# Kernel optimization log

Hardware: AMD Instinct MI355X
Metric: run time of the kernel (lower is better)

Reference implementation:

```python
import jax, jax.numpy as jnp
import numpy as np

N, D, E, H = 16384, 1024, 4, 4096
TEMP = 1.0

def setup_inputs() -> dict:
    key = jax.random.key(0)
    ks = jax.random.split(key, 6)
    s_in = 1.0 / np.sqrt(D)
    s_h = 1.0 / np.sqrt(H)
    s_g = 1.0 / np.sqrt(2 * D)
    return {
        "q": jax.random.normal(ks[0], (N, D), jnp.float32),
        "k": jax.random.normal(ks[1], (N, D), jnp.float32),
        "W1": jax.random.normal(ks[2], (E, D, H), jnp.float32) * s_in,
        "b1": jnp.zeros((E, H), jnp.float32),
        "W2": jax.random.normal(ks[3], (E, H, D), jnp.float32) * s_h,
        "b2": jnp.zeros((E, D), jnp.float32),
        "Wg": jax.random.normal(ks[4], (2 * D, 4), jnp.float32) * s_g,
        "bg": jnp.zeros((4,), jnp.float32),
    }

def reference(q, k, W1, b1, W2, b2, Wg, bg):
    # Run all E experts on the same tokens via batched GEMMs.
    h = jax.nn.relu(jnp.einsum('nd,edh->neh', q, W1) + b1)        # [N,E,H]
    q_pred = jnp.einsum('neh,ehd->ned', h, W2) + b2               # [N,E,D]
    # Gate: Linear(dim*2 -> 4) on concat(q,k), softmax over experts.
    logits = (jnp.concatenate([q, k], axis=-1) @ Wg + bg) / TEMP  # [N,4]
    gate = jax.nn.softmax(logits, axis=-1)                        # [N,E]
    return jnp.einsum('ned,ne->nd', q_pred, gate)                 # [N,D]
```

## Files before the change

### kernel.cpp

```cpp
#include <hip/hip_runtime.h>
#include <hip/hip_bf16.h>

#define N_TOK 16384
#define DIM   1024
#define NEXP  4
#define HID   4096
#define CHK   8192

typedef __attribute__((ext_vector_type(8))) short short8;
typedef __attribute__((ext_vector_type(4))) short short4v;
typedef __attribute__((ext_vector_type(4))) float float4v;

static __device__ __forceinline__ short f2bf(float f) {
  __hip_bfloat16 h = __float2bfloat16(f);
  return *reinterpret_cast<short*>(&h);
}

#define GLOAD_LDS16(gsrc, ldst)                                                            \
  __builtin_amdgcn_global_load_lds((const __attribute__((address_space(1))) void*)(gsrc),  \
                                   (__attribute__((address_space(3))) void*)(ldst), 16, 0, 0)

__global__ void gatecvt_kernel(const float* __restrict__ q, const float* __restrict__ k,
                               const float* __restrict__ Wg, const float* __restrict__ bg,
                               float* __restrict__ gate, short* __restrict__ qb) {
  const int wave = threadIdx.x >> 6, lane = threadIdx.x & 63;
  const int n = blockIdx.x * 4 + wave;
  const float* qr = q + (size_t)n * DIM;
  const float* kr = k + (size_t)n * DIM;
  short* qbr = qb + (size_t)n * DIM;
  float s0 = 0.f, s1 = 0.f, s2 = 0.f, s3 = 0.f;
#pragma unroll
  for (int it = 0; it < 4; ++it) {
    int d = it * 256 + lane * 4;
    float4 qv = *(const float4*)(qr + d);
    float4 kv = *(const float4*)(kr + d);
    short4v o;
    o[0] = f2bf(qv.x); o[1] = f2bf(qv.y); o[2] = f2bf(qv.z); o[3] = f2bf(qv.w);
    *(short4v*)(qbr + d) = o;
    const float xq[4] = {qv.x, qv.y, qv.z, qv.w};
    const float xk[4] = {kv.x, kv.y, kv.z, kv.w};
#pragma unroll
    for (int j = 0; j < 4; ++j) {
      float4 w = *(const float4*)(Wg + (size_t)(d + j) * 4);
      s0 += xq[j] * w.x; s1 += xq[j] * w.y; s2 += xq[j] * w.z; s3 += xq[j] * w.w;
      float4 w2 = *(const float4*)(Wg + (size_t)(DIM + d + j) * 4);
      s0 += xk[j] * w2.x; s1 += xk[j] * w2.y; s2 += xk[j] * w2.z; s3 += xk[j] * w2.w;
    }
  }
  for (int off = 32; off; off >>= 1) {
    s0 += __shfl_xor(s0, off);
    s1 += __shfl_xor(s1, off);
    s2 += __shfl_xor(s2, off);
    s3 += __shfl_xor(s3, off);
  }
  if (lane == 0) {
    float l0 = s0 + bg[0], l1 = s1 + bg[1], l2 = s2 + bg[2], l3 = s3 + bg[3];
    float m = fmaxf(fmaxf(l0, l1), fmaxf(l2, l3));
    float e0 = expf(l0 - m), e1 = expf(l1 - m), e2 = expf(l2 - m), e3 = expf(l3 - m);
    float inv = 1.f / (e0 + e1 + e2 + e3);
    float4 g; g.x = e0 * inv; g.y = e1 * inv; g.z = e2 * inv; g.w = e3 * inv;
    *(float4*)(gate + (size_t)n * 4) = g;
  }
}

__global__ void transpose_bf16_kernel(const float* __restrict__ in, short* __restrict__ out,
                                      int R, int C) {
  __shared__ float tile[64][65];
  const size_t eoff = (size_t)blockIdx.z * (size_t)R * C;
  const float* src = in + eoff;
  short* dst = out + eoff;
  const int r0 = blockIdx.y * 64, c0 = blockIdx.x * 64;
  const int tc = threadIdx.x & 63, tr = threadIdx.x >> 6;
#pragma unroll
  for (int p = 0; p < 16; ++p) {
    int r = p * 4 + tr;
    tile[r][tc] = src[(size_t)(r0 + r) * C + (c0 + tc)];
  }
  __syncthreads();
#pragma unroll
  for (int p = 0; p < 16; ++p) {
    int i = p * 4 + tr;
    dst[(size_t)(c0 + i) * R + (r0 + tc)] = f2bf(tile[tc][i]);
  }
}

template <int MODE>
__device__ __forceinline__ void gemm_body(short* sA, short* sB,
                                          const short* __restrict__ A, const short* __restrict__ Bt,
                                          int K, int NTM, int NTN, int bid,
                                          const float* __restrict__ bias,
                                          const float* __restrict__ gate4,
                                          short* __restrict__ OutB, float* __restrict__ FOut,
                                          int ldc, int accumulate) {
  int tile_m, tile_n;
  {
    const int m_own = NTM >> 3;
    const int xcd = bid & 7;
    const int idx = bid >> 3;
    const int mgrp = (m_own < 8) ? m_own : 8;
    const int per = mgrp * 4;
    const int pos = idx % per;
    const int chunk = idx / per;
    const int ml = pos % mgrp;
    const int nl = pos / mgrp;
    const int nchunks = NTN >> 2;
    const int nc = chunk % nchunks;
    const int mg2 = chunk / nchunks;
    tile_m = xcd * m_own + mg2 * mgrp + ml;
    tile_n = nc * 4 + nl;
  }
  const int m0 = tile_m * 128;
  const int n0 = tile_n * 128;

  const int t = threadIdx.x;
  const int lane = t & 63;
  const int wave = t >> 6;
  const int wm = (wave >> 1) * 64;
  const int wn = (wave & 1) * 64;
  const int r16 = lane & 15;
  const int kg = lane >> 4;

  float4v acc[4][4];
#pragma unroll
  for (int m = 0; m < 4; ++m)
#pragma unroll
    for (int n = 0; n < 4; ++n) acc[m][n] = (float4v)0.0f;

  for (int k0 = 0; k0 < K; k0 += 64) {
#pragma unroll
    for (int i = 0; i < 4; ++i) {
      int c = i * 256 + t;
      int row = c >> 3;
      int jc = (c & 7) ^ (row & 7);
      GLOAD_LDS16(A + (size_t)(m0 + row) * K + k0 + jc * 8, &sA[c * 8]);
      GLOAD_LDS16(Bt + (size_t)(n0 + row) * K + k0 + jc * 8, &sB[c * 8]);
    }
    __syncthreads();
#pragma unroll
    for (int kk = 0; kk < 2; ++kk) {
      short8 af[4], bfr[4];
#pragma unroll
      for (int m = 0; m < 4; ++m) {
        int row = wm + m * 16 + r16;
        int jc = (kk * 4 + kg) ^ (row & 7);
        af[m] = *(const short8*)&sA[row * 64 + jc * 8];
      }
#pragma unroll
      for (int n = 0; n < 4; ++n) {
        int row = wn + n * 16 + r16;
        int jc = (kk * 4 + kg) ^ (row & 7);
        bfr[n] = *(const short8*)&sB[row * 64 + jc * 8];
      }
#pragma unroll
      for (int m = 0; m < 4; ++m)
#pragma unroll
        for (int n = 0; n < 4; ++n)
          acc[m][n] = __builtin_amdgcn_mfma_f32_16x16x32_bf16(af[m], bfr[n], acc[m][n], 0, 0, 0);
    }
    __syncthreads();
  }

#pragma unroll
  for (int m = 0; m < 4; ++m) {
    int rbase = m0 + wm + m * 16 + kg * 4;
#pragma unroll
    for (int n = 0; n < 4; ++n) {
      int col = n0 + wn + n * 16 + r16;
      float bcol = bias[col];
#pragma unroll
      for (int r = 0; r < 4; ++r) {
        int grow = rbase + r;
        float g = gate4[(size_t)grow * 4];
        float v = acc[m][n][r];
        if (MODE == 1) {
          v += bcol;
          v = fmaxf(v, 0.f);
          v *= g;
          OutB[(size_t)grow * ldc + col] = f2bf(v);
        } else {
          v += g * bcol;
          size_t oi = (size_t)grow * ldc + col;
          if (accumulate) v += FOut[oi];
          FOut[oi] = v;
        }
      }
    }
  }
}

__global__ __launch_bounds__(256, 2)
void fused_kernel(const short* __restrict__ g1A, const short* __restrict__ g1B,
                  const float* __restrict__ g1bias, const float* __restrict__ g1gate,
                  short* __restrict__ g1out,
                  const short* __restrict__ g2A, const short* __restrict__ g2B,
                  const float* __restrict__ g2bias, const float* __restrict__ g2gate,
                  float* __restrict__ g2out, int g2accum, int g2n) {
  __shared__ short sA[128 * 64];
  __shared__ short sB[128 * 64];
  if ((int)blockIdx.x < g2n) {
    gemm_body<2>(sA, sB, g2A, g2B, HID, CHK / 128, DIM / 128, blockIdx.x,
                 g2bias, g2gate, nullptr, g2out, DIM, g2accum);
  } else {
    gemm_body<1>(sA, sB, g1A, g1B, DIM, CHK / 128, HID / 128, blockIdx.x - g2n,
                 g1bias, g1gate, g1out, nullptr, HID, 0);
  }
}

template <int MODE>
__global__ __launch_bounds__(256, 2)
void gemm_kernel(const short* __restrict__ A, const short* __restrict__ Bt, int K, int NTN,
                 const float* __restrict__ bias, const float* __restrict__ gate4,
                 short* __restrict__ OutB, float* __restrict__ FOut, int ldc, int accumulate) {
  __shared__ short sA[128 * 64];
  __shared__ short sB[128 * 64];
  gemm_body<MODE>(sA, sB, A, Bt, K, gridDim.x / NTN, NTN, blockIdx.x,
                  bias, gate4, OutB, FOut, ldc, accumulate);
}

extern "C" void kernel_launch(void* const* d_in, const int* in_sizes, int n_in,
                              void* d_out, int out_size, void* d_ws, size_t ws_size,
                              hipStream_t stream) {
  const float* q  = (const float*)d_in[0];
  const float* k  = (const float*)d_in[1];
  const float* W1 = (const float*)d_in[2];
  const float* b1 = (const float*)d_in[3];
  const float* W2 = (const float*)d_in[4];
  const float* b2 = (const float*)d_in[5];
  const float* Wg = (const float*)d_in[6];
  const float* bg = (const float*)d_in[7];
  float* out = (float*)d_out;

  char* ws = (char*)d_ws;
  size_t off = 0;
  float* gate = (float*)(ws + off); off += (size_t)N_TOK * 4 * sizeof(float);
  short* qb   = (short*)(ws + off); off += (size_t)N_TOK * DIM * 2;
  short* W1t  = (short*)(ws + off); off += (size_t)NEXP * (size_t)DIM * HID * 2;
  short* W2t  = (short*)(ws + off); off += (size_t)NEXP * (size_t)HID * DIM * 2;
  const size_t fixed = off;

  gatecvt_kernel<<<dim3(N_TOK / 4), dim3(256), 0, stream>>>(q, k, Wg, bg, gate, qb);
  transpose_bf16_kernel<<<dim3(HID / 64, DIM / 64, NEXP), dim3(256), 0, stream>>>(W1, W1t, DIM, HID);
  transpose_bf16_kernel<<<dim3(DIM / 64, HID / 64, NEXP), dim3(256), 0, stream>>>(W2, W2t, HID, DIM);

  size_t avail = (ws_size > fixed) ? ws_size - fixed : 0;
  const size_t hs_half = (size_t)CHK * HID * 2;

  if (2 * hs_half <= avail) {
    short* HsA = (short*)(ws + fixed);
    short* HsB = (short*)(ws + fixed + hs_half);
    short* hs[2] = {HsA, HsB};
    const int G1BLK = (CHK / 128) * (HID / 128);
    const int G2BLK = (CHK / 128) * (DIM / 128);

    fused_kernel<<<dim3(G1BLK), dim3(256), 0, stream>>>(
        qb, W1t, b1, gate, HsA,
        nullptr, nullptr, nullptr, nullptr, nullptr, 0, 0);
    for (int s = 0; s < 7; ++s) {
      const int c1 = (s + 1) & 1, e1 = (s + 1) >> 1;
      const int c2 = s & 1,       e2 = s >> 1;
      fused_kernel<<<dim3(G2BLK + G1BLK), dim3(256), 0, stream>>>(
          qb + (size_t)c1 * CHK * DIM, W1t + (size_t)e1 * HID * DIM,
          b1 + (size_t)e1 * HID, gate + (size_t)c1 * CHK * 4 + e1, hs[c1],
          hs[c2], W2t + (size_t)e2 * DIM * HID,
          b2 + (size_t)e2 * DIM, gate + (size_t)c2 * CHK * 4 + e2,
          out + (size_t)c2 * CHK * DIM, (e2 > 0) ? 1 : 0, G2BLK);
    }
    fused_kernel<<<dim3(G2BLK), dim3(256), 0, stream>>>(
        nullptr, nullptr, nullptr, nullptr, nullptr,
        hs[1], W2t + (size_t)3 * DIM * HID, b2 + (size_t)3 * DIM,
        gate + (size_t)CHK * 4 + 3, out + (size_t)CHK * DIM, 1, G2BLK);
  } else {
    short* Hs = (short*)(ws + fixed);
    long long mc = (long long)(avail / ((size_t)HID * 2));
    mc &= ~127LL;
    if (mc < 128) mc = 128;
    if (mc > N_TOK) mc = N_TOK;
    for (int cb = 0; cb < N_TOK; cb += (int)mc) {
      int rows = (N_TOK - cb < (int)mc) ? (N_TOK - cb) : (int)mc;
      for (int e = 0; e < NEXP; ++e) {
        gemm_kernel<1><<<dim3((rows / 128) * (HID / 128)), dim3(256), 0, stream>>>(
            qb + (size_t)cb * DIM, W1t + (size_t)e * HID * DIM, DIM, HID / 128,
            b1 + (size_t)e * HID, gate + (size_t)cb * 4 + e, Hs, nullptr, HID, 0);
        gemm_kernel<2><<<dim3((rows / 128) * (DIM / 128)), dim3(256), 0, stream>>>(
            Hs, W2t + (size_t)e * DIM * HID, HID, DIM / 128,
            b2 + (size_t)e * DIM, gate + (size_t)cb * 4 + e, nullptr,
            out + (size_t)cb * DIM, DIM, e > 0);
      }
    }
  }
}
```

Measured before the change: 1.277 ms.

## Merge prep kernels and overlap W2 transpose with first GEMM1 launch

Folds the gate/convert kernel and the W1 transpose into one prep launch. The W2 transpose blocks are appended to the first fused GEMM1 launch so that weight conversion runs alongside the first up-projection instead of before it. Shared memory is unified into one buffer reused as the transpose tile. This removes two launches and a serialization point. The cost is extra branching, and transpose blocks compete for CUs with GEMM blocks.

```diff
diff --git a/kernel.cpp b/kernel.cpp
--- a/kernel.cpp
+++ b/kernel.cpp
@@ -20,11 +20,36 @@
   __builtin_amdgcn_global_load_lds((const __attribute__((address_space(1))) void*)(gsrc),  \
                                    (__attribute__((address_space(3))) void*)(ldst), 16, 0, 0)
 
-__global__ void gatecvt_kernel(const float* __restrict__ q, const float* __restrict__ k,
-                               const float* __restrict__ Wg, const float* __restrict__ bg,
-                               float* __restrict__ gate, short* __restrict__ qb) {
+
+__device__ __forceinline__ void transpose_body(const float* __restrict__ src0,
+                                               short* __restrict__ dst0, int R, int C,
+                                               int bx, int by, int bz, float (*tile)[65]) {
+  const size_t eoff = (size_t)bz * (size_t)R * C;
+  const float* src = src0 + eoff;
+  short* dst = dst0 + eoff;
+  const int r0 = by * 64, c0 = bx * 64;
+  const int tc = threadIdx.x & 63, tr = threadIdx.x >> 6;
+#pragma unroll
+  for (int p = 0; p < 16; ++p) {
+    int r = p * 4 + tr;
+    tile[r][tc] = src[(size_t)(r0 + r) * C + (c0 + tc)];
+  }
+  __syncthreads();
+#pragma unroll
+  for (int p = 0; p < 16; ++p) {
+    int i = p * 4 + tr;
+    dst[(size_t)(c0 + i) * R + (r0 + tc)] = f2bf(tile[tc][i]);
+  }
+}
+
+__device__ __forceinline__ void gatecvt_body(const float* __restrict__ q,
+                                             const float* __restrict__ k,
+                                             const float* __restrict__ Wg,
+                                             const float* __restrict__ bg,
+                                             float* __restrict__ gate, short* __restrict__ qb,
+                                             int bid) {
   const int wave = threadIdx.x >> 6, lane = threadIdx.x & 63;
-  const int n = blockIdx.x * 4 + wave;
+  const int n = bid * 4 + wave;
   const float* qr = q + (size_t)n * DIM;
   const float* kr = k + (size_t)n * DIM;
   short* qbr = qb + (size_t)n * DIM;
@@ -63,24 +88,24 @@
   }
 }
 
-__global__ void transpose_bf16_kernel(const float* __restrict__ in, short* __restrict__ out,
-                                      int R, int C) {
+__global__ __launch_bounds__(256)
+void prep_kernel(const float* __restrict__ q, const float* __restrict__ k,
+                 const float* __restrict__ Wg, const float* __restrict__ bg,
+                 float* __restrict__ gate, short* __restrict__ qb,
+                 const float* __restrict__ W1, short* __restrict__ W1t,
+                 const float* __restrict__ W2, short* __restrict__ W2t) {
   __shared__ float tile[64][65];
-  const size_t eoff = (size_t)blockIdx.z * (size_t)R * C;
-  const float* src = in + eoff;
-  short* dst = out + eoff;
-  const int r0 = blockIdx.y * 64, c0 = blockIdx.x * 64;
-  const int tc = threadIdx.x & 63, tr = threadIdx.x >> 6;
-#pragma unroll
-  for (int p = 0; p < 16; ++p) {
-    int r = p * 4 + tr;
-    tile[r][tc] = src[(size_t)(r0 + r) * C + (c0 + tc)];
-  }
-  __syncthreads();
-#pragma unroll
-  for (int p = 0; p < 16; ++p) {
-    int i = p * 4 + tr;
-    dst[(size_t)(c0 + i) * R + (r0 + tc)] = f2bf(tile[tc][i]);
+  const int bid = blockIdx.x;
+  if (bid < N_TOK / 4) {
+    gatecvt_body(q, k, Wg, bg, gate, qb, bid);
+  } else if (bid < N_TOK / 4 + (HID / 64) * (DIM / 64) * NEXP) {
+    int i = bid - N_TOK / 4;
+    transpose_body(W1, W1t, DIM, HID, i % (HID / 64), (i / (HID / 64)) % (DIM / 64),
+                   i / ((HID / 64) * (DIM / 64)), tile);
+  } else {
+    int i = bid - N_TOK / 4 - (HID / 64) * (DIM / 64) * NEXP;
+    transpose_body(W2, W2t, HID, DIM, i % (DIM / 64), (i / (DIM / 64)) % (HID / 64),
+                   i / ((DIM / 64) * (HID / 64)), tile);
   }
 }
 
@@ -194,15 +219,20 @@
                   short* __restrict__ g1out,
                   const short* __restrict__ g2A, const short* __restrict__ g2B,
                   const float* __restrict__ g2bias, const float* __restrict__ g2gate,
-                  float* __restrict__ g2out, int g2accum, int g2n) {
-  __shared__ short sA[128 * 64];
-  __shared__ short sB[128 * 64];
-  if ((int)blockIdx.x < g2n) {
-    gemm_body<2>(sA, sB, g2A, g2B, HID, CHK / 128, DIM / 128, blockIdx.x,
+                  float* __restrict__ g2out, int g2accum, int g2n, int g1n,
+                  const float* __restrict__ tsrc, short* __restrict__ tdst) {
+  __shared__ short smem[2 * 128 * 64];
+  const int bid = blockIdx.x;
+  if (bid < g2n) {
+    gemm_body<2>(smem, smem + 8192, g2A, g2B, HID, CHK / 128, DIM / 128, bid,
                  g2bias, g2gate, nullptr, g2out, DIM, g2accum);
+  } else if (bid < g2n + g1n) {
+    gemm_body<1>(smem, smem + 8192, g1A, g1B, DIM, CHK / 128, HID / 128, bid - g2n,
+                 g1bias, g1gate, g1out, nullptr, HID, 0);
   } else {
-    gemm_body<1>(sA, sB, g1A, g1B, DIM, CHK / 128, HID / 128, blockIdx.x - g2n,
-                 g1bias, g1gate, g1out, nullptr, HID, 0);
+    int i = bid - g2n - g1n;
+    transpose_body(tsrc, tdst, HID, DIM, i % (DIM / 64), (i / (DIM / 64)) % (HID / 64),
+                   i / ((DIM / 64) * (HID / 64)), (float(*)[65])smem);
   }
 }
 
@@ -211,9 +241,8 @@
 void gemm_kernel(const short* __restrict__ A, const short* __restrict__ Bt, int K, int NTN,
                  const float* __restrict__ bias, const float* __restrict__ gate4,
                  short* __restrict__ OutB, float* __restrict__ FOut, int ldc, int accumulate) {
-  __shared__ short sA[128 * 64];
-  __shared__ short sB[128 * 64];
-  gemm_body<MODE>(sA, sB, A, Bt, K, gridDim.x / NTN, NTN, blockIdx.x,
+  __shared__ short smem[2 * 128 * 64];
+  gemm_body<MODE>(smem, smem + 8192, A, Bt, K, gridDim.x / NTN, NTN, blockIdx.x,
                   bias, gate4, OutB, FOut, ldc, accumulate);
 }
 
@@ -238,23 +267,26 @@
   short* W2t  = (short*)(ws + off); off += (size_t)NEXP * (size_t)HID * DIM * 2;
   const size_t fixed = off;
 
-  gatecvt_kernel<<<dim3(N_TOK / 4), dim3(256), 0, stream>>>(q, k, Wg, bg, gate, qb);
-  transpose_bf16_kernel<<<dim3(HID / 64, DIM / 64, NEXP), dim3(256), 0, stream>>>(W1, W1t, DIM, HID);
-  transpose_bf16_kernel<<<dim3(DIM / 64, HID / 64, NEXP), dim3(256), 0, stream>>>(W2, W2t, HID, DIM);
+  const int GATEB = N_TOK / 4;
+  const int W1TB  = (HID / 64) * (DIM / 64) * NEXP;
+  const int W2TB  = (DIM / 64) * (HID / 64) * NEXP;
 
   size_t avail = (ws_size > fixed) ? ws_size - fixed : 0;
   const size_t hs_half = (size_t)CHK * HID * 2;
 
   if (2 * hs_half <= avail) {
+    prep_kernel<<<dim3(GATEB + W1TB), dim3(256), 0, stream>>>(
+        q, k, Wg, bg, gate, qb, W1, W1t, W2, W2t);
+
     short* HsA = (short*)(ws + fixed);
     short* HsB = (short*)(ws + fixed + hs_half);
     short* hs[2] = {HsA, HsB};
     const int G1BLK = (CHK / 128) * (HID / 128);
     const int G2BLK = (CHK / 128) * (DIM / 128);
 
-    fused_kernel<<<dim3(G1BLK), dim3(256), 0, stream>>>(
+    fused_kernel<<<dim3(G1BLK + W2TB), dim3(256), 0, stream>>>(
         qb, W1t, b1, gate, HsA,
-        nullptr, nullptr, nullptr, nullptr, nullptr, 0, 0);
+        nullptr, nullptr, nullptr, nullptr, nullptr, 0, 0, G1BLK, W2, W2t);
     for (int s = 0; s < 7; ++s) {
       const int c1 = (s + 1) & 1, e1 = (s + 1) >> 1;
       const int c2 = s & 1,       e2 = s >> 1;
@@ -263,13 +295,17 @@
           b1 + (size_t)e1 * HID, gate + (size_t)c1 * CHK * 4 + e1, hs[c1],
           hs[c2], W2t + (size_t)e2 * DIM * HID,
           b2 + (size_t)e2 * DIM, gate + (size_t)c2 * CHK * 4 + e2,
-          out + (size_t)c2 * CHK * DIM, (e2 > 0) ? 1 : 0, G2BLK);
+          out + (size_t)c2 * CHK * DIM, (e2 > 0) ? 1 : 0, G2BLK, G1BLK,
+          nullptr, nullptr);
     }
     fused_kernel<<<dim3(G2BLK), dim3(256), 0, stream>>>(
         nullptr, nullptr, nullptr, nullptr, nullptr,
         hs[1], W2t + (size_t)3 * DIM * HID, b2 + (size_t)3 * DIM,
-        gate + (size_t)CHK * 4 + 3, out + (size_t)CHK * DIM, 1, G2BLK);
+        gate + (size_t)CHK * 4 + 3, out + (size_t)CHK * DIM, 1, G2BLK, 0,
+        nullptr, nullptr);
   } else {
+    prep_kernel<<<dim3(GATEB + W1TB + W2TB), dim3(256), 0, stream>>>(
+        q, k, Wg, bg, gate, qb, W1, W1t, W2, W2t);
     short* Hs = (short*)(ws + fixed);
     long long mc = (long long)(avail / ((size_t)HID * 2));
     mc &= ~127LL;
```

New measurement: 1.265 ms. Within noise of the previous version (-0.9%).
